# Kernel optimization log

Hardware: AMD Instinct MI355X
Metric: run time of the kernel (lower is better)

## Reference

```python
import jax, jax.numpy as jnp
import numpy as np

N_QUBITS = 12
N_LAYERS = 3
N_CHUNKS = 12
CHUNK = 4
BATCH = 2048


def _u3(theta, phi, lam):
    # PennyLane U3 = [[cos(t/2), -e^{i l} sin(t/2)], [e^{i p} sin(t/2), e^{i(p+l)} cos(t/2)]]
    ct = jnp.cos(theta / 2).astype(jnp.complex64)
    st = jnp.sin(theta / 2).astype(jnp.complex64)
    ep = jnp.exp(1j * phi.astype(jnp.complex64))
    el = jnp.exp(1j * lam.astype(jnp.complex64))
    return jnp.stack([jnp.stack([ct, -el * st]), jnp.stack([ep * st, ep * el * ct])])


def _apply_1q(state, U, w):
    # state: (2,)*N_QUBITS
    s = jnp.moveaxis(state, w, 0)
    s = jnp.tensordot(U, s, axes=1)
    return jnp.moveaxis(s, 0, w)


def _apply_cnot(state, c, t):
    s = jnp.moveaxis(state, (c, t), (0, 1))
    s = jnp.stack([s[0], jnp.flip(s[1], axis=0)], axis=0)
    return jnp.moveaxis(s, (0, 1), (c, t))


def _circuit(params):
    # params: [N_CHUNKS, 3] -> expval PauliZ per wire, shape [N_QUBITS]
    state = jnp.zeros((2,) * N_QUBITS, jnp.complex64).at[(0,) * N_QUBITS].set(1.0)
    for _ in range(N_LAYERS):
        for i in range(N_CHUNKS):
            state = _apply_1q(state, _u3(params[i, 0], params[i, 1], params[i, 2]), i)
        for i in range(N_QUBITS):
            state = _apply_cnot(state, i, (i + 1) % N_QUBITS)
    p = jnp.abs(state) ** 2
    sign = jnp.array([1.0, -1.0], p.dtype)
    zs = []
    for i in range(N_QUBITS):
        marg = p.sum(axis=tuple(a for a in range(N_QUBITS) if a != i))
        zs.append(jnp.dot(marg, sign))
    return jnp.stack(zs)


def setup_inputs() -> dict:
    key = jax.random.key(0)
    ks = jax.random.split(key, 7)
    return {
        "x": jax.random.normal(ks[0], (BATCH, 48), jnp.float32),
        "reupload_weights": jax.random.normal(ks[1], (N_CHUNKS, 3, CHUNK), jnp.float32) * 0.1,
        "reupload_bias": jax.random.normal(ks[2], (N_CHUNKS, 3), jnp.float32) * 0.1,
        "w1": jax.random.normal(ks[3], (64, N_QUBITS), jnp.float32) * 0.1,
        "b1": jax.random.normal(ks[4], (64,), jnp.float32) * 0.1,
        "w2": jax.random.normal(ks[5], (256, 64), jnp.float32) * 0.1,
        "b2": jax.random.normal(ks[6], (256,), jnp.float32) * 0.1,
    }


def reference(x, reupload_weights, reupload_bias, w1, b1, w2, b2):
    chunks = x.reshape(-1, N_CHUNKS, CHUNK)  # [B, 12, 4]
    # per-chunk affine map: [12,3,4] @ [B,12,4] -> [B,12,3]
    params = jnp.einsum("cpk,bck->bcp", reupload_weights, chunks) + reupload_bias
    qz = jax.vmap(_circuit)(params)  # [B, 12]
    h = jax.nn.relu(qz @ w1.T + b1)
    return h @ w2.T + b2
```

## Files before the change

kernel.cpp:

```cpp
#include <hip/hip_runtime.h>
#include <hip/hip_fp16.h>
#include <math.h>

typedef _Float16 half8 __attribute__((ext_vector_type(8)));
typedef float f32x4 __attribute__((ext_vector_type(4)));

__device__ __forceinline__ int pfx4(int x) {
    return (x ^ (x << 1) ^ (x << 2) ^ (x << 3)) & 15;
}

__global__ __attribute__((amdgpu_flat_work_group_size(256, 256)))
void qparam_kernel(const float* __restrict__ x, const float* __restrict__ rw,
                   const float* __restrict__ rb, float* __restrict__ uo, int total)
{
    const int g = blockIdx.x * 256 + threadIdx.x;
    if (g >= total) return;
    const int c = g % 12;
    const float4 xv = ((const float4*)x)[g];
    float prm[3];
    #pragma unroll
    for (int p = 0; p < 3; ++p) {
        const float4 wv = ((const float4*)rw)[c * 3 + p];
        prm[p] = rb[c * 3 + p] + wv.x * xv.x + wv.y * xv.y + wv.z * xv.z + wv.w * xv.w;
    }
    float st_, ct_; sincosf(0.5f * prm[0], &st_, &ct_);
    float sp_, cp_; sincosf(prm[1], &sp_, &cp_);
    float sl_, cl_; sincosf(prm[2], &sl_, &cl_);
    const float cpl = cp_ * cl_ - sp_ * sl_;
    const float spl = sp_ * cl_ + cp_ * sl_;
    ((float4*)uo)[g * 2]     = make_float4(ct_, 0.0f, -cl_ * st_, -sl_ * st_);
    ((float4*)uo)[g * 2 + 1] = make_float4(cp_ * st_, sp_ * st_, cpl * ct_, spl * ct_);
}

__global__ __attribute__((amdgpu_flat_work_group_size(256, 256), amdgpu_waves_per_eu(4, 4)))
void qreup_kernel(const float* __restrict__ uin,
                  const float* __restrict__ w1, const float* __restrict__ b1,
                  const float* __restrict__ w2, const float* __restrict__ b2,
                  float* __restrict__ out)
{
    __shared__ __align__(16) char lds[32768];
    char* const wl = lds;

    const int t = threadIdx.x;
    const int b = blockIdx.x;
    const float* __restrict__ ub = uin + b * 96;
    const int l15 = t & 15, q = (t >> 4) & 3, wv = t >> 6;

    {
        const int mp = t >> 4, mm = t & 15;
        #pragma unroll
        for (int g = 0; g < 3; ++g) {
            const float* p0 = ub + g * 32 + ((mp & 1) * 4 + (mm & 1) * 2);
            float wr = p0[0], wi = p0[1];
            #pragma unroll
            for (int bq = 1; bq < 4; ++bq) {
                const float* p = ub + g * 32 + bq * 8 + ((mp >> bq) & 1) * 4 + ((mm >> bq) & 1) * 2;
                const float br = p[0], bi = p[1];
                const float nr = wr * br - wi * bi, ni = wr * bi + wi * br;
                wr = nr; wi = ni;
            }
            const _Float16 hr = (_Float16)wr, hi_ = (_Float16)wi;
            const _Float16 lr = (_Float16)(wr - (float)hr), li = (_Float16)(wi - (float)hi_);
            union { _Float16 h[2]; unsigned int u; } ph, pl_;
            ph.h[0] = hr;  ph.h[1] = hi_;
            pl_.h[0] = lr; pl_.h[1] = li;
            *(unsigned int*)(wl + g * 2048 +        mp * 64 + mm * 4) = ph.u;
            *(unsigned int*)(wl + g * 2048 + 1024 + mp * 64 + mm * 4) = pl_.u;
        }
    }
    __syncthreads();

    half8 ArH[3], ArL[3], AiH[3], AiL[3];
    #pragma unroll
    for (int g = 0; g < 3; ++g) {
        #pragma unroll
        for (int hl = 0; hl < 2; ++hl) {
            int4 raw = *(const int4*)(wl + g * 2048 + hl * 1024 + l15 * 64 + q * 16);
            int re4[4], im4[4];
            int rr[4] = {raw.x, raw.y, raw.z, raw.w};
            #pragma unroll
            for (int i = 0; i < 4; ++i) {
                re4[i] = rr[i] ^ 0x80000000;
                im4[i] = (int)(((unsigned)rr[i] >> 16) | ((unsigned)rr[i] << 16));
            }
            half8 hre, him;
            __builtin_memcpy(&hre, re4, 16);
            __builtin_memcpy(&him, im4, 16);
            if (hl == 0) { ArH[g] = hre; AiH[g] = him; }
            else         { ArL[g] = hre; AiL[g] = him; }
        }
    }

    const int Ml = pfx4(l15);
    const int piL = (Ml >> 3) & 1;

    float A0 = 0.f, AT0 = 0.f, AT01 = 0.f, AR0 = 0.f, AR01 = 0.f;
    char* rbuf = lds;
    char* wbuf = lds + 16384;

    #pragma unroll 1
    for (int L = 0; L < 3; ++L) {
        if (L) __syncthreads();
        #pragma unroll
        for (int T = 0; T < 4; ++T) {
            const int tt = wv * 4 + T;
            half8 bfr;
            if (L == 0) {
                half8 z = {};
                if (t == 0 && T == 0) z[0] = (_Float16)1.0f;
                bfr = z;
            } else {
                const int nu = 16 * tt + l15;
                const int al = ((l15 >> 1) & 1) | ((((l15 >> 1) ^ (l15 >> 2)) & 1) << 1);
                const int be = ((tt >> 1) ^ (tt >> 2)) & 1;
                int4 raw = *(const int4*)(rbuf + 64 * (nu ^ be) + 16 * (q ^ al));
                if (tt & 8) {
                    int tmp = raw.x; raw.x = raw.y; raw.y = tmp;
                    tmp = raw.z; raw.z = raw.w; raw.w = tmp;
                }
                __builtin_memcpy(&bfr, &raw, 16);
            }
            f32x4 cre = {0.f,0.f,0.f,0.f}, cim = {0.f,0.f,0.f,0.f};
            cre = __builtin_amdgcn_mfma_f32_16x16x32_f16(ArH[0], bfr, cre, 0, 0, 0);
            cre = __builtin_amdgcn_mfma_f32_16x16x32_f16(ArL[0], bfr, cre, 0, 0, 0);
            cim = __builtin_amdgcn_mfma_f32_16x16x32_f16(AiH[0], bfr, cim, 0, 0, 0);
            cim = __builtin_amdgcn_mfma_f32_16x16x32_f16(AiL[0], bfr, cim, 0, 0, 0);
            const int als = q ^ ((tt >> 1) & 3);
            const int bes = (tt ^ q) & 1;
            const int D = 4 * (l15 ^ (als << 2));
            #pragma unroll
            for (int r = 0; r < 4; ++r) {
                const int nu = (4 * q + r) + 16 * tt;
                __half2 hp = __floats2half2_rn(cre[r], cim[r]);
                *(unsigned int*)(wbuf + 64 * (nu ^ bes) + D) = *(unsigned int*)&hp;
            }
        }
        { char* tmp = rbuf; rbuf = wbuf; wbuf = tmp; }

        __syncthreads();
        #pragma unroll
        for (int T = 0; T < 4; ++T) {
            const int tt = wv * 4 + T;
            const int nu = tt + 16 * l15;
            const int al = ((tt >> 2) & 3) ^ ((l15 >> 1) & 3);
            const int be = (l15 ^ (tt >> 2)) & 1;
            int4 raw = *(const int4*)(rbuf + 64 * (nu ^ be) + 16 * (q ^ al));
            half8 bfr; __builtin_memcpy(&bfr, &raw, 16);
            f32x4 cre = {0.f,0.f,0.f,0.f}, cim = {0.f,0.f,0.f,0.f};
            cre = __builtin_amdgcn_mfma_f32_16x16x32_f16(ArH[1], bfr, cre, 0, 0, 0);
            cre = __builtin_amdgcn_mfma_f32_16x16x32_f16(ArL[1], bfr, cre, 0, 0, 0);
            cim = __builtin_amdgcn_mfma_f32_16x16x32_f16(AiH[1], bfr, cim, 0, 0, 0);
            cim = __builtin_amdgcn_mfma_f32_16x16x32_f16(AiL[1], bfr, cim, 0, 0, 0);
            const int als = ((tt >> 1) & 3) ^ q;
            const int bes = q & 1;
            const int D = 4 * (l15 ^ (als << 2));
            #pragma unroll
            for (int r = 0; r < 4; ++r) {
                const int nu2 = tt + 16 * (4 * q + r);
                __half2 hp = __floats2half2_rn(cre[r], cim[r]);
                *(unsigned int*)(wbuf + 64 * (nu2 ^ bes) + D) = *(unsigned int*)&hp;
            }
        }
        { char* tmp = rbuf; rbuf = wbuf; wbuf = tmp; }

        __syncthreads();
        #pragma unroll
        for (int T = 0; T < 4; ++T) {
            const int tt = wv * 4 + T;
            const int nu = l15 + 16 * tt;
            const int al = ((l15 >> 1) & 3) ^ ((tt >> 2) & 3);
            const int be = (tt >> 2) & 1;
            int4 raw = *(const int4*)(rbuf + 64 * (nu ^ be) + 16 * (q ^ al));
            half8 bfr; __builtin_memcpy(&bfr, &raw, 16);
            f32x4 cre = {0.f,0.f,0.f,0.f}, cim = {0.f,0.f,0.f,0.f};
            cre = __builtin_amdgcn_mfma_f32_16x16x32_f16(ArH[2], bfr, cre, 0, 0, 0);
            cre = __builtin_amdgcn_mfma_f32_16x16x32_f16(ArL[2], bfr, cre, 0, 0, 0);
            cim = __builtin_amdgcn_mfma_f32_16x16x32_f16(AiH[2], bfr, cim, 0, 0, 0);
            cim = __builtin_amdgcn_mfma_f32_16x16x32_f16(AiL[2], bfr, cim, 0, 0, 0);
            if (L < 2) {
                const int taub = pfx4(tt);
                const int lowH = (piL ? 15 : 0) ^ taub;
                const int s    = (lowH >> 3) & 1;
                const int als  = ((lowH >> 1) & 1) | ((((lowH >> 1) ^ (lowH >> 2)) & 1) << 1);
                const int bes  = q & 1;
                const int D = 4 * (Ml ^ (als << 2));
                #pragma unroll
                for (int r = 0; r < 4; ++r) {
                    const int rho = pfx4(4 * q + r);
                    const int H = lowH | (((s ? 15 : 0) ^ rho) << 4);
                    __half2 hp = __floats2half2_rn(cre[r], cim[r]);
                    *(unsigned int*)(wbuf + 64 * (H ^ bes) + D) = *(unsigned int*)&hp;
                }
            } else {
                const int sT0 = T & 1, sT01 = (T ^ (T >> 1)) & 1;
                #pragma unroll
                for (int r = 0; r < 4; ++r) {
                    const float pr = cre[r] * cre[r] + cim[r] * cim[r];
                    A0 += pr;
                    AT0  += sT0 ? -pr : pr;
                    AT01 += sT01 ? -pr : pr;
                    AR0  += (sT01 ^ (r & 1)) ? -pr : pr;
                    AR01 += (sT01 ^ ((r ^ (r >> 1)) & 1)) ? -pr : pr;
                }
            }
        }
        { char* tmp = rbuf; rbuf = wbuf; wbuf = tmp; }
    }

    const int pl = __popc(l15) & 1;
    const int wv0 = wv & 1, wv1 = (wv >> 1) & 1, wv01 = wv0 ^ wv1;
    const int q0 = q & 1, q1 = (q >> 1) & 1;
    float zp[12];
    zp[1] = (__popc(l15 & 3) & 1) ? -A0 : A0;
    zp[2] = (__popc(l15 & 7) & 1) ? -A0 : A0;
    zp[3] = pl ? -A0 : A0;
    zp[4] = pl ? -AT0 : AT0;
    zp[5] = pl ? -AT01 : AT01;
    zp[6] = (pl ^ wv0) ? -AT01 : AT01;
    zp[7] = (pl ^ wv0 ^ wv1) ? -AT01 : AT01;
    zp[8] = (pl ^ wv01) ? -AR0 : AR0;
    zp[9] = (pl ^ wv01) ? -AR01 : AR01;
    zp[10] = (pl ^ wv01 ^ q0) ? -AR01 : AR01;
    zp[11] = (pl ^ wv01 ^ q0 ^ q1) ? -AR01 : AR01;
    zp[0]  = ((l15 & 1) ^ pl ^ wv01 ^ q0 ^ q1) ? -AR01 : AR01;

    #pragma unroll
    for (int i = 0; i < 12; ++i) {
        float vv = zp[i];
        #pragma unroll
        for (int off = 32; off > 0; off >>= 1)
            vv += __shfl_xor(vv, off, 64);
        zp[i] = vv;
    }

    __syncthreads();
    float* stf  = (float*)lds;
    float* zred = stf;
    float* qzs  = stf + 48;
    float* hbuf = stf + 64;

    if ((t & 63) == 0) {
        #pragma unroll
        for (int i = 0; i < 12; ++i) zred[wv * 12 + i] = zp[i];
    }
    __syncthreads();
    if (t < 12)
        qzs[t] = zred[t] + zred[12 + t] + zred[24 + t] + zred[36 + t];
    __syncthreads();

    if (t < 64) {
        float acc = b1[t];
        #pragma unroll
        for (int i = 0; i < 12; ++i) acc += qzs[i] * w1[t * 12 + i];
        hbuf[t] = fmaxf(acc, 0.0f);
    }
    __syncthreads();
    float acc = b2[t];
    #pragma unroll 4
    for (int k4 = 0; k4 < 16; ++k4) {
        const float4 wvv = ((const float4*)w2)[t * 16 + k4];
        acc += wvv.x * hbuf[k4 * 4 + 0] + wvv.y * hbuf[k4 * 4 + 1]
             + wvv.z * hbuf[k4 * 4 + 2] + wvv.w * hbuf[k4 * 4 + 3];
    }
    out[b * 256 + t] = acc;
}

extern "C" void kernel_launch(void* const* d_in, const int* in_sizes, int n_in,
                              void* d_out, int out_size, void* d_ws, size_t ws_size,
                              hipStream_t stream) {
    const float* x  = (const float*)d_in[0];
    const float* rw = (const float*)d_in[1];
    const float* rb = (const float*)d_in[2];
    const float* w1 = (const float*)d_in[3];
    const float* b1 = (const float*)d_in[4];
    const float* w2 = (const float*)d_in[5];
    const float* b2 = (const float*)d_in[6];
    float* out = (float*)d_out;
    float* uws = (float*)d_ws;

    const int batch = in_sizes[0] / 48;
    const int total = batch * 12;
    qparam_kernel<<<(total + 255) / 256, 256, 0, stream>>>(x, rw, rb, uws, total);
    qreup_kernel<<<batch, 256, 0, stream>>>(uws, w1, b1, w2, b2, out);
}
```

Measured before the change: 98.38 us.

## Fuse gate-parameter kernel into main kernel and restructure LDS swizzled stores

Computes the per-chunk U3 gate matrices inside the main kernel: 12 threads per block write them to a spare LDS region. This removes the separate qparam launch and the global workspace round trip. It also rewrites the swizzled half2 stores in two MFMA stages, turning the XOR-based row index into a conditional swap of register values paired with fixed row offsets. In exchange, each block spends a short serial prologue on sincos in a few threads, with an extra barrier before the gate products.

```diff
diff --git a/kernel.cpp b/kernel.cpp
--- a/kernel.cpp
+++ b/kernel.cpp
@@ -9,31 +9,9 @@
     return (x ^ (x << 1) ^ (x << 2) ^ (x << 3)) & 15;
 }
 
-__global__ __attribute__((amdgpu_flat_work_group_size(256, 256)))
-void qparam_kernel(const float* __restrict__ x, const float* __restrict__ rw,
-                   const float* __restrict__ rb, float* __restrict__ uo, int total)
-{
-    const int g = blockIdx.x * 256 + threadIdx.x;
-    if (g >= total) return;
-    const int c = g % 12;
-    const float4 xv = ((const float4*)x)[g];
-    float prm[3];
-    #pragma unroll
-    for (int p = 0; p < 3; ++p) {
-        const float4 wv = ((const float4*)rw)[c * 3 + p];
-        prm[p] = rb[c * 3 + p] + wv.x * xv.x + wv.y * xv.y + wv.z * xv.z + wv.w * xv.w;
-    }
-    float st_, ct_; sincosf(0.5f * prm[0], &st_, &ct_);
-    float sp_, cp_; sincosf(prm[1], &sp_, &cp_);
-    float sl_, cl_; sincosf(prm[2], &sl_, &cl_);
-    const float cpl = cp_ * cl_ - sp_ * sl_;
-    const float spl = sp_ * cl_ + cp_ * sl_;
-    ((float4*)uo)[g * 2]     = make_float4(ct_, 0.0f, -cl_ * st_, -sl_ * st_);
-    ((float4*)uo)[g * 2 + 1] = make_float4(cp_ * st_, sp_ * st_, cpl * ct_, spl * ct_);
-}
-
 __global__ __attribute__((amdgpu_flat_work_group_size(256, 256), amdgpu_waves_per_eu(4, 4)))
-void qreup_kernel(const float* __restrict__ uin,
+void qreup_kernel(const float* __restrict__ x, const float* __restrict__ rw,
+                  const float* __restrict__ rb,
                   const float* __restrict__ w1, const float* __restrict__ b1,
                   const float* __restrict__ w2, const float* __restrict__ b2,
                   float* __restrict__ out)
@@ -43,18 +21,36 @@
 
     const int t = threadIdx.x;
     const int b = blockIdx.x;
-    const float* __restrict__ ub = uin + b * 96;
     const int l15 = t & 15, q = (t >> 4) & 3, wv = t >> 6;
+
+    float* const uL = (float*)(lds + 16384);
+    if (t < 12) {
+        const float4 xv = ((const float4*)x)[b * 12 + t];
+        float prm[3];
+        #pragma unroll
+        for (int p = 0; p < 3; ++p) {
+            const float4 wvv = ((const float4*)rw)[t * 3 + p];
+            prm[p] = rb[t * 3 + p] + wvv.x * xv.x + wvv.y * xv.y + wvv.z * xv.z + wvv.w * xv.w;
+        }
+        float st_, ct_; sincosf(0.5f * prm[0], &st_, &ct_);
+        float sp_, cp_; sincosf(prm[1], &sp_, &cp_);
+        float sl_, cl_; sincosf(prm[2], &sl_, &cl_);
+        const float cpl = cp_ * cl_ - sp_ * sl_;
+        const float spl = sp_ * cl_ + cp_ * sl_;
+        ((float4*)uL)[t * 2]     = make_float4(ct_, 0.0f, -cl_ * st_, -sl_ * st_);
+        ((float4*)uL)[t * 2 + 1] = make_float4(cp_ * st_, sp_ * st_, cpl * ct_, spl * ct_);
+    }
+    __syncthreads();
 
     {
         const int mp = t >> 4, mm = t & 15;
         #pragma unroll
         for (int g = 0; g < 3; ++g) {
-            const float* p0 = ub + g * 32 + ((mp & 1) * 4 + (mm & 1) * 2);
+            const float* p0 = uL + g * 32 + ((mp & 1) * 4 + (mm & 1) * 2);
             float wr = p0[0], wi = p0[1];
             #pragma unroll
             for (int bq = 1; bq < 4; ++bq) {
-                const float* p = ub + g * 32 + bq * 8 + ((mp >> bq) & 1) * 4 + ((mm >> bq) & 1) * 2;
+                const float* p = uL + g * 32 + bq * 8 + ((mp >> bq) & 1) * 4 + ((mm >> bq) & 1) * 2;
                 const float br = p[0], bi = p[1];
                 const float nr = wr * br - wi * bi, ni = wr * bi + wi * br;
                 wr = nr; wi = ni;
@@ -128,37 +124,60 @@
             const int als = q ^ ((tt >> 1) & 3);
             const int bes = (tt ^ q) & 1;
             const int D = 4 * (l15 ^ (als << 2));
+            unsigned p4[4];
             #pragma unroll
             for (int r = 0; r < 4; ++r) {
-                const int nu = (4 * q + r) + 16 * tt;
                 __half2 hp = __floats2half2_rn(cre[r], cim[r]);
-                *(unsigned int*)(wbuf + 64 * (nu ^ bes) + D) = *(unsigned int*)&hp;
-            }
+                p4[r] = *(unsigned int*)&hp;
+            }
+            char* rowb = wbuf + 64 * (4 * q + 16 * tt) + D;
+            const unsigned s0 = bes ? p4[1] : p4[0];
+            const unsigned s1 = bes ? p4[0] : p4[1];
+            const unsigned s2 = bes ? p4[3] : p4[2];
+            const unsigned s3 = bes ? p4[2] : p4[3];
+            *(unsigned int*)(rowb      ) = s0;
+            *(unsigned int*)(rowb +  64) = s1;
+            *(unsigned int*)(rowb + 128) = s2;
+            *(unsigned int*)(rowb + 192) = s3;
         }
         { char* tmp = rbuf; rbuf = wbuf; wbuf = tmp; }
 
         __syncthreads();
         #pragma unroll
-        for (int T = 0; T < 4; ++T) {
-            const int tt = wv * 4 + T;
-            const int nu = tt + 16 * l15;
-            const int al = ((tt >> 2) & 3) ^ ((l15 >> 1) & 3);
-            const int be = (l15 ^ (tt >> 2)) & 1;
-            int4 raw = *(const int4*)(rbuf + 64 * (nu ^ be) + 16 * (q ^ al));
-            half8 bfr; __builtin_memcpy(&bfr, &raw, 16);
-            f32x4 cre = {0.f,0.f,0.f,0.f}, cim = {0.f,0.f,0.f,0.f};
-            cre = __builtin_amdgcn_mfma_f32_16x16x32_f16(ArH[1], bfr, cre, 0, 0, 0);
-            cre = __builtin_amdgcn_mfma_f32_16x16x32_f16(ArL[1], bfr, cre, 0, 0, 0);
-            cim = __builtin_amdgcn_mfma_f32_16x16x32_f16(AiH[1], bfr, cim, 0, 0, 0);
-            cim = __builtin_amdgcn_mfma_f32_16x16x32_f16(AiL[1], bfr, cim, 0, 0, 0);
-            const int als = ((tt >> 1) & 3) ^ q;
+        for (int Tp = 0; Tp < 2; ++Tp) {
+            unsigned pe[4], po[4];
+            #pragma unroll
+            for (int hf = 0; hf < 2; ++hf) {
+                const int T = Tp * 2 + hf;
+                const int tt = wv * 4 + T;
+                const int nu = tt + 16 * l15;
+                const int al = ((tt >> 2) & 3) ^ ((l15 >> 1) & 3);
+                const int be = (l15 ^ (tt >> 2)) & 1;
+                int4 raw = *(const int4*)(rbuf + 64 * (nu ^ be) + 16 * (q ^ al));
+                half8 bfr; __builtin_memcpy(&bfr, &raw, 16);
+                f32x4 cre = {0.f,0.f,0.f,0.f}, cim = {0.f,0.f,0.f,0.f};
+                cre = __builtin_amdgcn_mfma_f32_16x16x32_f16(ArH[1], bfr, cre, 0, 0, 0);
+                cre = __builtin_amdgcn_mfma_f32_16x16x32_f16(ArL[1], bfr, cre, 0, 0, 0);
+                cim = __builtin_amdgcn_mfma_f32_16x16x32_f16(AiH[1], bfr, cim, 0, 0, 0);
+                cim = __builtin_amdgcn_mfma_f32_16x16x32_f16(AiL[1], bfr, cim, 0, 0, 0);
+                #pragma unroll
+                for (int r = 0; r < 4; ++r) {
+                    __half2 hp = __floats2half2_rn(cre[r], cim[r]);
+                    if (hf == 0) pe[r] = *(unsigned int*)&hp;
+                    else         po[r] = *(unsigned int*)&hp;
+                }
+            }
+            const int tt0 = wv * 4 + Tp * 2;
+            const int als = ((tt0 >> 1) & 3) ^ q;
             const int bes = q & 1;
             const int D = 4 * (l15 ^ (als << 2));
             #pragma unroll
             for (int r = 0; r < 4; ++r) {
-                const int nu2 = tt + 16 * (4 * q + r);
-                __half2 hp = __floats2half2_rn(cre[r], cim[r]);
-                *(unsigned int*)(wbuf + 64 * (nu2 ^ bes) + D) = *(unsigned int*)&hp;
+                char* base = wbuf + 64 * (tt0 + 16 * (4 * q + r)) + D;
+                const unsigned lo = bes ? po[r] : pe[r];
+                const unsigned hi = bes ? pe[r] : po[r];
+                *(unsigned int*)(base     ) = lo;
+                *(unsigned int*)(base + 64) = hi;
             }
         }
         { char* tmp = rbuf; rbuf = wbuf; wbuf = tmp; }
@@ -276,10 +295,8 @@
     const float* w2 = (const float*)d_in[5];
     const float* b2 = (const float*)d_in[6];
     float* out = (float*)d_out;
-    float* uws = (float*)d_ws;
+    (void)d_ws; (void)ws_size;
 
     const int batch = in_sizes[0] / 48;
-    const int total = batch * 12;
-    qparam_kernel<<<(total + 255) / 256, 256, 0, stream>>>(x, rw, rb, uws, total);
-    qreup_kernel<<<batch, 256, 0, stream>>>(uws, w1, b1, w2, b2, out);
+    qreup_kernel<<<batch, 256, 0, stream>>>(x, rw, rb, w1, b1, w2, b2, out);
 }
```

After: 96.81 us. No clear change (-1.6%).
